# Kernel optimization log

Hardware: AMD Instinct MI355X
Metric: run time of the kernel (lower is better)

The kernel has to match this reference:

```python
import jax, jax.numpy as jnp
import numpy as np

NUM_HEADS = 16
HEAD_DIM = 64

def setup_inputs() -> dict:
    key = jax.random.key(0)
    k1, k2, k3 = jax.random.split(key, 3)
    B, S, H = 2, 2048, 1024
    inner = NUM_HEADS * HEAD_DIM  # 1024
    x = jax.random.normal(k1, (B, S, H), dtype=jnp.float32)
    w_qkv = jax.random.normal(k2, (H, 3 * inner), dtype=jnp.float32) * (1.0 / np.sqrt(H))
    b_qkv = jnp.zeros((3 * inner,), dtype=jnp.float32)
    w_out = jax.random.normal(k3, (inner, H), dtype=jnp.float32) * (1.0 / np.sqrt(inner))
    b_out = jnp.zeros((H,), dtype=jnp.float32)
    return {"x": x, "w_qkv": w_qkv, "b_qkv": b_qkv, "w_out": w_out, "b_out": b_out}

def reference(x, w_qkv, b_qkv, w_out, b_out):
    B, S, H = x.shape
    nh, hd = NUM_HEADS, HEAD_DIM
    qkv = x @ w_qkv + b_qkv                      # [B,S,3*nh*hd]
    qkv = qkv.reshape(B, S, 3, nh, hd)
    qkv = jnp.transpose(qkv, (2, 0, 3, 1, 4))    # [3,B,nh,S,hd]
    q, k, v = qkv[0], qkv[1], qkv[2]
    scale = jnp.sqrt(jnp.asarray(hd, dtype=x.dtype))
    attn = jnp.einsum('bhqd,bhkd->bhqk', q, k) / scale  # [B,nh,S,S]
    attn = jax.nn.softmax(attn, axis=-1)
    out = jnp.einsum('bhqk,bhkd->bhqd', attn, v)        # [B,nh,S,hd]
    out = jnp.transpose(out, (0, 2, 1, 3)).reshape(B, S, nh * hd)
    out = out @ w_out + b_out                    # [B,S,H]
    return out
```

## Files before the change

### kernel.cpp

```cpp
#include <hip/hip_runtime.h>
#include <stdint.h>

typedef short bf16x8 __attribute__((ext_vector_type(8)));
typedef float f32x4 __attribute__((ext_vector_type(4)));

#if __has_builtin(__builtin_amdgcn_exp2f)
#define EXP2F(x) __builtin_amdgcn_exp2f(x)
#else
#define EXP2F(x) exp2f(x)
#endif

#define QSCALE 0.18033688011112042f

__device__ __forceinline__ unsigned short f2bf(float f) {
  unsigned u = __float_as_uint(f);
  u += 0x7fffu + ((u >> 16) & 1u);
  return (unsigned short)(u >> 16);
}

__device__ __forceinline__ unsigned cvtpk(float lo, float hi) {
  unsigned r;
  asm("v_cvt_pk_bf16_f32 %0, %1, %2" : "=v"(r) : "v"(lo), "v"(hi));
  return r;
}

__device__ __forceinline__ void pl32(unsigned& a, unsigned& b) {
  asm("v_permlane32_swap_b32 %0, %1" : "+v"(a), "+v"(b));
}
__device__ __forceinline__ void pl16(unsigned& a, unsigned& b) {
  asm("v_permlane16_swap_b32 %0, %1" : "+v"(a), "+v"(b));
}

__device__ __forceinline__ void gld16(const ushort* g, ushort* l) {
  __builtin_amdgcn_global_load_lds(
      (__attribute__((address_space(1))) void*)g,
      (__attribute__((address_space(3))) void*)l, 16, 0, 0);
}

__global__ __launch_bounds__(256) void k_prep(
    const float* __restrict__ x, ushort* __restrict__ xb,
    const float* __restrict__ wqkv, ushort* __restrict__ wqkvT,
    const float* __restrict__ wout, ushort* __restrict__ woutT) {
  __shared__ float tl[32][33];
  const int t = threadIdx.x;
  const int blk = blockIdx.x;
  if (blk < 2048) {
    int i = (blk * 256 + t) * 8;
    float4 a = *(const float4*)(x + i);
    float4 b = *(const float4*)(x + i + 4);
    union { ushort u[8]; uint4 q; } r;
    r.u[0] = f2bf(a.x); r.u[1] = f2bf(a.y); r.u[2] = f2bf(a.z); r.u[3] = f2bf(a.w);
    r.u[4] = f2bf(b.x); r.u[5] = f2bf(b.y); r.u[6] = f2bf(b.z); r.u[7] = f2bf(b.w);
    *(uint4*)(xb + i) = r.q;
    return;
  }
  const float* in; ushort* out; int C, bx, by;
  if (blk < 5120) {
    int b = blk - 2048; bx = b % 96; by = b / 96;
    in = wqkv; out = wqkvT; C = 3072;
  } else {
    int b = blk - 5120; bx = b & 31; by = b >> 5;
    in = wout; out = woutT; C = 1024;
  }
  const int R = 1024;
  {
    int r = t >> 3, c4 = (t & 7) * 4;
    float4 v = *(const float4*)(in + (size_t)(by * 32 + r) * C + bx * 32 + c4);
    tl[r][c4] = v.x; tl[r][c4 + 1] = v.y; tl[r][c4 + 2] = v.z; tl[r][c4 + 3] = v.w;
  }
  __syncthreads();
  {
    int c = t >> 3, r4 = (t & 7) * 4;
    union { ushort u[4]; uint2 q; } o;
    o.u[0] = f2bf(tl[r4][c]);     o.u[1] = f2bf(tl[r4 + 1][c]);
    o.u[2] = f2bf(tl[r4 + 2][c]); o.u[3] = f2bf(tl[r4 + 3][c]);
    *(uint2*)(out + (size_t)(bx * 32 + c) * R + by * 32 + r4) = o.q;
  }
}

__global__ __launch_bounds__(256, 2) void k_gemm_qkv(
    const ushort* __restrict__ A, const ushort* __restrict__ Bt,
    const float* __restrict__ bias, ushort* __restrict__ Q,
    ushort* __restrict__ Ko, ushort* __restrict__ Vt) {
  __shared__ ushort As[2][128 * 32];
  __shared__ ushort Bs[2][128 * 32];
  const int t = threadIdx.x;
  const int lane = t & 63, wid = t >> 6;
  const int wr = wid >> 1, wc = wid & 1;
  const int rt = blockIdx.y, ct = blockIdx.x;

  const int srow = t >> 2, sslot = t & 3;
  const ushort* ga = A + (size_t)(rt * 128 + srow) * 1024 + sslot * 8;
  const ushort* gb = Bt + (size_t)(ct * 128 + srow) * 1024 + sslot * 8;

  f32x4 acc[4][4];
#pragma unroll
  for (int m = 0; m < 4; ++m)
#pragma unroll
    for (int n = 0; n < 4; ++n) acc[m][n] = (f32x4){0.f, 0.f, 0.f, 0.f};

  int aidx[4], bidx[4];
#pragma unroll
  for (int m = 0; m < 4; ++m) {
    int ra = wr * 64 + m * 16 + (lane & 15);
    aidx[m] = ra * 32 + ((lane >> 4) << 3);
    int rb = wc * 64 + m * 16 + (lane & 15);
    bidx[m] = rb * 32 + ((lane >> 4) << 3);
  }

  gld16(ga, &As[0][t * 8]); gld16(ga + 65536, &As[0][2048 + t * 8]);
  gld16(gb, &Bs[0][t * 8]); gld16(gb + 65536, &Bs[0][2048 + t * 8]);
  __syncthreads();

  int cur = 0;
  for (int kt = 0; kt < 32; ++kt) {
    if (kt < 31) {
      const ushort* ga2 = ga + (kt + 1) * 32;
      const ushort* gb2 = gb + (kt + 1) * 32;
      gld16(ga2, &As[cur ^ 1][t * 8]); gld16(ga2 + 65536, &As[cur ^ 1][2048 + t * 8]);
      gld16(gb2, &Bs[cur ^ 1][t * 8]); gld16(gb2 + 65536, &Bs[cur ^ 1][2048 + t * 8]);
    }
    bf16x8 af[4], bfv[4];
#pragma unroll
    for (int m = 0; m < 4; ++m) af[m] = *(const bf16x8*)&As[cur][aidx[m]];
#pragma unroll
    for (int n = 0; n < 4; ++n) bfv[n] = *(const bf16x8*)&Bs[cur][bidx[n]];
#pragma unroll
    for (int m = 0; m < 4; ++m)
#pragma unroll
      for (int n = 0; n < 4; ++n)
        acc[m][n] = __builtin_amdgcn_mfma_f32_16x16x32_bf16(af[m], bfv[n], acc[m][n], 0, 0, 0);
    __syncthreads();
    cur ^= 1;
  }

  const int colb = ct * 128 + wc * 64;
  const int rowb = rt * 128 + wr * 64;
#pragma unroll
  for (int n = 0; n < 4; ++n) {
    int col = colb + n * 16 + (lane & 15);
    float bv = bias[col];
    int three = col >> 10, hx = (col >> 6) & 15, d = col & 63;
    if (three == 2) {
#pragma unroll
      for (int m = 0; m < 4; ++m) {
        int r0 = rowb + m * 16 + ((lane >> 4) << 2);
        int b = r0 >> 11, s0 = r0 & 2047;
        int s0p = (s0 & ~56) | (((s0 >> 3) ^ d) & 7) << 3;
        union { ushort u[4]; uint2 q; } o;
#pragma unroll
        for (int r = 0; r < 4; ++r) o.u[r] = f2bf(acc[m][n][r] + bv);
        *(uint2*)&Vt[(size_t)(b * 16 + hx) * 131072 + (size_t)d * 2048 + s0p] = o.q;
      }
    } else if (three == 1) {
#pragma unroll
      for (int m = 0; m < 4; ++m) {
        int r0 = rowb + m * 16 + ((lane >> 4) << 2);
#pragma unroll
        for (int r = 0; r < 4; ++r) {
          int row = r0 + r;
          int b = row >> 11, s = row & 2047;
          int dp = (d & 7) | ((((d >> 3) ^ s) & 7) << 3);
          Ko[(size_t)((b * 16 + hx) * 2048 + s) * 64 + dp] = f2bf(acc[m][n][r] + bv);
        }
      }
    } else {
#pragma unroll
      for (int m = 0; m < 4; ++m) {
        int r0 = rowb + m * 16 + ((lane >> 4) << 2);
#pragma unroll
        for (int r = 0; r < 4; ++r) {
          int row = r0 + r;
          int b = row >> 11, s = row & 2047;
          Q[(size_t)((b * 16 + hx) * 2048 + s) * 64 + d] = f2bf((acc[m][n][r] + bv) * QSCALE);
        }
      }
    }
  }
}

__global__ __launch_bounds__(256, 2) void k_gemm_out(
    const ushort* __restrict__ A, const ushort* __restrict__ Bt,
    const float* __restrict__ bias, float* __restrict__ Out) {
  __shared__ ushort As[2][64 * 32];
  __shared__ ushort Bs[2][128 * 32];
  const int t = threadIdx.x;
  const int lane = t & 63, wid = t >> 6;
  const int wr = wid >> 1, wc = wid & 1;
  const int rt = blockIdx.y, ct = blockIdx.x;

  const int srow = t >> 2, sslot = t & 3;
  const ushort* ga = A + (size_t)(rt * 64 + srow) * 1024 + sslot * 8;
  const ushort* gb = Bt + (size_t)(ct * 128 + srow) * 1024 + sslot * 8;

  f32x4 acc[2][4];
#pragma unroll
  for (int m = 0; m < 2; ++m)
#pragma unroll
    for (int n = 0; n < 4; ++n) acc[m][n] = (f32x4){0.f, 0.f, 0.f, 0.f};

  int aidx[2], bidx[4];
#pragma unroll
  for (int m = 0; m < 2; ++m) {
    int ra = wr * 32 + m * 16 + (lane & 15);
    aidx[m] = ra * 32 + ((lane >> 4) << 3);
  }
#pragma unroll
  for (int n = 0; n < 4; ++n) {
    int rb = wc * 64 + n * 16 + (lane & 15);
    bidx[n] = rb * 32 + ((lane >> 4) << 3);
  }

  gld16(ga, &As[0][t * 8]);
  gld16(gb, &Bs[0][t * 8]); gld16(gb + 65536, &Bs[0][2048 + t * 8]);
  __syncthreads();

  int cur = 0;
  for (int kt = 0; kt < 32; ++kt) {
    if (kt < 31) {
      const ushort* ga2 = ga + (kt + 1) * 32;
      const ushort* gb2 = gb + (kt + 1) * 32;
      gld16(ga2, &As[cur ^ 1][t * 8]);
      gld16(gb2, &Bs[cur ^ 1][t * 8]); gld16(gb2 + 65536, &Bs[cur ^ 1][2048 + t * 8]);
    }
    bf16x8 af[2], bfv[4];
#pragma unroll
    for (int m = 0; m < 2; ++m) af[m] = *(const bf16x8*)&As[cur][aidx[m]];
#pragma unroll
    for (int n = 0; n < 4; ++n) bfv[n] = *(const bf16x8*)&Bs[cur][bidx[n]];
#pragma unroll
    for (int m = 0; m < 2; ++m)
#pragma unroll
      for (int n = 0; n < 4; ++n)
        acc[m][n] = __builtin_amdgcn_mfma_f32_16x16x32_bf16(af[m], bfv[n], acc[m][n], 0, 0, 0);
    __syncthreads();
    cur ^= 1;
  }

  const int colb = ct * 128 + wc * 64;
  const int rowb = rt * 64 + wr * 32;
#pragma unroll
  for (int n = 0; n < 4; ++n) {
    int col = colb + n * 16 + (lane & 15);
    float bv = bias[col];
#pragma unroll
    for (int m = 0; m < 2; ++m) {
      int r0 = rowb + m * 16 + ((lane >> 4) << 2);
#pragma unroll
      for (int r = 0; r < 4; ++r)
        Out[(size_t)(r0 + r) * 1024 + col] = acc[m][n][r] + bv;
    }
  }
}

#define QKT_COMPUTE(KSRC, SD)                                                 \
  {                                                                           \
    _Pragma("unroll")                                                         \
    for (int cb = 0; cb < 2; ++cb)                                            \
      _Pragma("unroll")                                                       \
      for (int n = 0; n < 4; ++n) SD[cb][n] = (f32x4){0.f, 0.f, 0.f, 0.f};    \
    __builtin_amdgcn_s_setprio(1);                                            \
    _Pragma("unroll")                                                         \
    for (int kk = 0; kk < 2; ++kk)                                            \
      _Pragma("unroll")                                                       \
      for (int n = 0; n < 4; ++n) {                                           \
        bf16x8 kf = *(const bf16x8*)&(KSRC)[kidx[n][kk]];                     \
        SD[0][n] = __builtin_amdgcn_mfma_f32_16x16x32_bf16(kf, qf[0][kk], SD[0][n], 0, 0, 0); \
        SD[1][n] = __builtin_amdgcn_mfma_f32_16x16x32_bf16(kf, qf[1][kk], SD[1][n], 0, 0, 0); \
      }                                                                       \
    __builtin_amdgcn_s_setprio(0);                                            \
  }

#define ATTN_ITER(T, SCUR, SNXT)                                              \
  {                                                                           \
    if ((T) < 30) {                                                           \
      _Pragma("unroll")                                                       \
      for (int i = 0; i < 2; ++i) {                                           \
        int row = (wid * 2 + i) * 8 + strow;                                  \
        gld16(&Kh[(size_t)(((T) + 2) * 64 + row) * 64 + stch],                \
              Kstg + (wid * 2 + i) * 512 + lane * 8);                         \
        gld16(&Vh[(size_t)row * 2048 + ((T) + 2) * 64 + stch],                \
              Vstg + (wid * 2 + i) * 512 + lane * 8);                         \
      }                                                                       \
    }                                                                         \
    if ((T) < 31) QKT_COMPUTE(Knxt, SNXT);                                    \
    uint2 W[2][4];                                                            \
    _Pragma("unroll")                                                         \
    for (int cb = 0; cb < 2; ++cb) {                                          \
      float ps = lpart[cb];                                                   \
      _Pragma("unroll")                                                       \
      for (int n = 0; n < 4; ++n) {                                           \
        float p0 = EXP2F(SCUR[cb][n][0] - 16.0f);                             \
        float p1 = EXP2F(SCUR[cb][n][1] - 16.0f);                             \
        float p2 = EXP2F(SCUR[cb][n][2] - 16.0f);                             \
        float p3 = EXP2F(SCUR[cb][n][3] - 16.0f);                             \
        ps += (p0 + p1) + (p2 + p3);                                          \
        W[cb][n].x = cvtpk(p0, p1);                                           \
        W[cb][n].y = cvtpk(p2, p3);                                           \
      }                                                                       \
      lpart[cb] = ps;                                                         \
    }                                                                         \
    __builtin_amdgcn_s_setprio(1);                                            \
    _Pragma("unroll")                                                         \
    for (int kk = 0; kk < 2; ++kk) {                                          \
      bf16x8 paf[2];                                                          \
      _Pragma("unroll")                                                       \
      for (int cb = 0; cb < 2; ++cb) {                                        \
        unsigned a0 = W[cb][2 * kk].x, b0 = W[cb][2 * kk + 1].x;              \
        pl32(a0, b0); pl16(a0, b0);                                           \
        unsigned a1 = W[cb][2 * kk].y, b1 = W[cb][2 * kk + 1].y;              \
        pl32(a1, b1); pl16(a1, b1);                                           \
        union { unsigned u[4]; bf16x8 v; } fr;                                \
        fr.u[0] = a0; fr.u[1] = a1; fr.u[2] = b0; fr.u[3] = b1;               \
        paf[cb] = fr.v;                                                       \
      }                                                                       \
      _Pragma("unroll")                                                       \
      for (int nd = 0; nd < 4; ++nd) {                                        \
        bf16x8 vf = *(const bf16x8*)&Vcur[kidx[nd][kk]];                      \
        oacc[0][nd] = __builtin_amdgcn_mfma_f32_16x16x32_bf16(paf[0], vf, oacc[0][nd], 0, 0, 0); \
        oacc[1][nd] = __builtin_amdgcn_mfma_f32_16x16x32_bf16(paf[1], vf, oacc[1][nd], 0, 0, 0); \
      }                                                                       \
    }                                                                         \
    __builtin_amdgcn_s_setprio(0);                                            \
    __syncthreads();                                                          \
    { ushort* tk = Kcur; Kcur = Knxt; Knxt = Kstg; Kstg = tk;                 \
      ushort* tv = Vcur; Vcur = Vnxt; Vnxt = Vstg; Vstg = tv; }               \
  }

__global__ __launch_bounds__(256, 2) void k_attn(const ushort* __restrict__ Qb,
                                                 const ushort* __restrict__ Kb,
                                                 const ushort* __restrict__ Vtb,
                                                 ushort* __restrict__ AO) {
  __shared__ ushort Ks[3][64 * 64];
  __shared__ ushort Vs[3][64 * 64];
  const int t = threadIdx.x, lane = t & 63, wid = t >> 6;
  const int c = lane & 15, g = lane >> 4;
  const int bh = blockIdx.y, qt = blockIdx.x;
  const ushort* Qh = Qb + (size_t)bh * 131072;
  const ushort* Kh = Kb + (size_t)bh * 131072;
  const ushort* Vh = Vtb + (size_t)bh * 131072;

  bf16x8 qf[2][2];
#pragma unroll
  for (int cb = 0; cb < 2; ++cb)
#pragma unroll
    for (int kk = 0; kk < 2; ++kk) {
      int row = qt * 128 + wid * 32 + cb * 16 + c;
      qf[cb][kk] = *(const bf16x8*)&Qh[row * 64 + kk * 32 + g * 8];
    }

  f32x4 oacc[2][4];
#pragma unroll
  for (int cb = 0; cb < 2; ++cb)
#pragma unroll
    for (int n = 0; n < 4; ++n) oacc[cb][n] = (f32x4){0.f, 0.f, 0.f, 0.f};
  float lpart[2] = {0.f, 0.f};

  const int strow = lane >> 3, stch = (lane & 7) * 8;

  int kidx[4][2];
#pragma unroll
  for (int n = 0; n < 4; ++n)
#pragma unroll
    for (int kk = 0; kk < 2; ++kk)
      kidx[n][kk] = (n * 16 + c) * 64 + (((kk * 4 + g) ^ (c & 7)) << 3);

  ushort *Kcur = &Ks[0][0], *Knxt = &Ks[1][0], *Kstg = &Ks[2][0];
  ushort *Vcur = &Vs[0][0], *Vnxt = &Vs[1][0], *Vstg = &Vs[2][0];

#pragma unroll
  for (int i = 0; i < 2; ++i) {
    int row = (wid * 2 + i) * 8 + strow;
    gld16(&Kh[(size_t)row * 64 + stch], Kcur + (wid * 2 + i) * 512 + lane * 8);
    gld16(&Vh[(size_t)row * 2048 + stch], Vcur + (wid * 2 + i) * 512 + lane * 8);
    gld16(&Kh[(size_t)(64 + row) * 64 + stch], Knxt + (wid * 2 + i) * 512 + lane * 8);
    gld16(&Vh[(size_t)row * 2048 + 64 + stch], Vnxt + (wid * 2 + i) * 512 + lane * 8);
  }
  __syncthreads();

  f32x4 sA[2][4], sB[2][4];
  QKT_COMPUTE(Kcur, sA);

  for (int kt = 0; kt < 32; kt += 2) {
    ATTN_ITER(kt, sA, sB);
    ATTN_ITER(kt + 1, sB, sA);
  }

  const int b = bh >> 4, h = bh & 15;
#pragma unroll
  for (int cb = 0; cb < 2; ++cb) {
    float lp = lpart[cb];
    lp += __shfl_xor(lp, 16);
    lp += __shfl_xor(lp, 32);
    float inv = 1.0f / lp;
    float invr[4];
#pragma unroll
    for (int r = 0; r < 4; ++r) invr[r] = __shfl(inv, (g << 2) + r);
#pragma unroll
    for (int nd = 0; nd < 4; ++nd) {
      int d = nd * 16 + c;
#pragma unroll
      for (int r = 0; r < 4; ++r) {
        int s = qt * 128 + wid * 32 + cb * 16 + (g << 2) + r;
        AO[(size_t)((b * 2048 + s) * 16 + h) * 64 + d] = f2bf(oacc[cb][nd][r] * invr[r]);
      }
    }
  }
}

extern "C" void kernel_launch(void* const* d_in, const int* in_sizes, int n_in,
                              void* d_out, int out_size, void* d_ws, size_t ws_size,
                              hipStream_t stream) {
  const float* x = (const float*)d_in[0];
  const float* w_qkv = (const float*)d_in[1];
  const float* b_qkv = (const float*)d_in[2];
  const float* w_out = (const float*)d_in[3];
  const float* b_out = (const float*)d_in[4];
  float* out = (float*)d_out;

  char* p = (char*)d_ws;
  ushort* xb = (ushort*)p;    p += (size_t)4096 * 1024 * 2;
  ushort* wqkvT = (ushort*)p; p += (size_t)3072 * 1024 * 2;
  ushort* woutT = (ushort*)p; p += (size_t)1024 * 1024 * 2;
  ushort* Qb = (ushort*)p;    p += (size_t)32 * 2048 * 64 * 2;
  ushort* Kb = (ushort*)p;    p += (size_t)32 * 2048 * 64 * 2;
  ushort* Vtb = (ushort*)p;   p += (size_t)32 * 2048 * 64 * 2;
  ushort* AO = xb;

  k_prep<<<6144, 256, 0, stream>>>(x, xb, w_qkv, wqkvT, w_out, woutT);
  k_gemm_qkv<<<dim3(24, 32), 256, 0, stream>>>(xb, wqkvT, b_qkv, Qb, Kb, Vtb);
  k_attn<<<dim3(16, 32), 256, 0, stream>>>(Qb, Kb, Vtb, AO);
  k_gemm_out<<<dim3(8, 64), 256, 0, stream>>>(AO, woutT, b_out, out);
}
```

Before: 109.5 us.

## Deepen LDS prefetch pipelines with vmcnt-gated barriers in GEMMs and attention

```diff
diff --git a/kernel.cpp b/kernel.cpp
--- a/kernel.cpp
+++ b/kernel.cpp
@@ -36,6 +36,14 @@
       (__attribute__((address_space(1))) void*)g,
       (__attribute__((address_space(3))) void*)l, 16, 0, 0);
 }
+
+#define VMBAR(N)                                          \
+  asm volatile("s_waitcnt vmcnt(" #N ")" ::: "memory");   \
+  __builtin_amdgcn_s_barrier();                           \
+  __builtin_amdgcn_sched_barrier(0);
+#define BARONLY                                           \
+  __builtin_amdgcn_s_barrier();                           \
+  __builtin_amdgcn_sched_barrier(0);
 
 __global__ __launch_bounds__(256) void k_prep(
     const float* __restrict__ x, ushort* __restrict__ xb,
@@ -78,12 +86,34 @@
   }
 }
 
+#define QKV_BODY(KT, ISSUE)                                                   \
+  {                                                                           \
+    if (ISSUE) {                                                              \
+      const ushort* ga2 = ga + ((KT) + 2) * 32;                               \
+      const ushort* gb2 = gb + ((KT) + 2) * 32;                               \
+      gld16(ga2, Astg + t * 8); gld16(ga2 + 65536, Astg + 2048 + t * 8);      \
+      gld16(gb2, Bstg + t * 8); gld16(gb2 + 65536, Bstg + 2048 + t * 8);      \
+    }                                                                         \
+    bf16x8 af[4], bfv[4];                                                     \
+    _Pragma("unroll")                                                         \
+    for (int m = 0; m < 4; ++m) af[m] = *(const bf16x8*)&Acur[aidx[m]];       \
+    _Pragma("unroll")                                                         \
+    for (int n = 0; n < 4; ++n) bfv[n] = *(const bf16x8*)&Bcur[bidx[n]];      \
+    _Pragma("unroll")                                                         \
+    for (int m = 0; m < 4; ++m)                                               \
+      _Pragma("unroll")                                                       \
+      for (int n = 0; n < 4; ++n)                                             \
+        acc[m][n] = __builtin_amdgcn_mfma_f32_16x16x32_bf16(af[m], bfv[n], acc[m][n], 0, 0, 0); \
+    { ushort* ta = Acur; Acur = Anxt; Anxt = Astg; Astg = ta;                 \
+      ushort* tb = Bcur; Bcur = Bnxt; Bnxt = Bstg; Bstg = tb; }               \
+  }
+
 __global__ __launch_bounds__(256, 2) void k_gemm_qkv(
     const ushort* __restrict__ A, const ushort* __restrict__ Bt,
     const float* __restrict__ bias, ushort* __restrict__ Q,
     ushort* __restrict__ Ko, ushort* __restrict__ Vt) {
-  __shared__ ushort As[2][128 * 32];
-  __shared__ ushort Bs[2][128 * 32];
+  __shared__ ushort As[3][128 * 32];
+  __shared__ ushort Bs[3][128 * 32];
   const int t = threadIdx.x;
   const int lane = t & 63, wid = t >> 6;
   const int wr = wid >> 1, wc = wid & 1;
@@ -108,31 +138,26 @@
     bidx[m] = rb * 32 + ((lane >> 4) << 3);
   }
 
-  gld16(ga, &As[0][t * 8]); gld16(ga + 65536, &As[0][2048 + t * 8]);
-  gld16(gb, &Bs[0][t * 8]); gld16(gb + 65536, &Bs[0][2048 + t * 8]);
-  __syncthreads();
-
-  int cur = 0;
-  for (int kt = 0; kt < 32; ++kt) {
-    if (kt < 31) {
-      const ushort* ga2 = ga + (kt + 1) * 32;
-      const ushort* gb2 = gb + (kt + 1) * 32;
-      gld16(ga2, &As[cur ^ 1][t * 8]); gld16(ga2 + 65536, &As[cur ^ 1][2048 + t * 8]);
-      gld16(gb2, &Bs[cur ^ 1][t * 8]); gld16(gb2 + 65536, &Bs[cur ^ 1][2048 + t * 8]);
-    }
-    bf16x8 af[4], bfv[4];
-#pragma unroll
-    for (int m = 0; m < 4; ++m) af[m] = *(const bf16x8*)&As[cur][aidx[m]];
-#pragma unroll
-    for (int n = 0; n < 4; ++n) bfv[n] = *(const bf16x8*)&Bs[cur][bidx[n]];
-#pragma unroll
-    for (int m = 0; m < 4; ++m)
-#pragma unroll
-      for (int n = 0; n < 4; ++n)
-        acc[m][n] = __builtin_amdgcn_mfma_f32_16x16x32_bf16(af[m], bfv[n], acc[m][n], 0, 0, 0);
-    __syncthreads();
-    cur ^= 1;
-  }
+  ushort *Acur = &As[0][0], *Anxt = &As[1][0], *Astg = &As[2][0];
+  ushort *Bcur = &Bs[0][0], *Bnxt = &Bs[1][0], *Bstg = &Bs[2][0];
+
+  gld16(ga, Acur + t * 8); gld16(ga + 65536, Acur + 2048 + t * 8);
+  gld16(gb, Bcur + t * 8); gld16(gb + 65536, Bcur + 2048 + t * 8);
+  {
+    const ushort* ga1 = ga + 32;
+    const ushort* gb1 = gb + 32;
+    gld16(ga1, Anxt + t * 8); gld16(ga1 + 65536, Anxt + 2048 + t * 8);
+    gld16(gb1, Bnxt + t * 8); gld16(gb1 + 65536, Bnxt + 2048 + t * 8);
+  }
+  VMBAR(4)
+
+  for (int kt = 0; kt < 30; ++kt) {
+    QKV_BODY(kt, true)
+    VMBAR(4)
+  }
+  QKV_BODY(30, false)
+  VMBAR(0)
+  QKV_BODY(31, false)
 
   const int colb = ct * 128 + wc * 64;
   const int rowb = rt * 128 + wr * 64;
@@ -179,11 +204,33 @@
   }
 }
 
+#define OUT_BODY(KT, ISSUE)                                                   \
+  {                                                                           \
+    if (ISSUE) {                                                              \
+      const ushort* ga2 = ga + ((KT) + 2) * 32;                               \
+      const ushort* gb2 = gb + ((KT) + 2) * 32;                               \
+      gld16(ga2, Astg + t * 8);                                               \
+      gld16(gb2, Bstg + t * 8); gld16(gb2 + 65536, Bstg + 2048 + t * 8);      \
+    }                                                                         \
+    bf16x8 af[2], bfv[4];                                                     \
+    _Pragma("unroll")                                                         \
+    for (int m = 0; m < 2; ++m) af[m] = *(const bf16x8*)&Acur[aidx[m]];       \
+    _Pragma("unroll")                                                         \
+    for (int n = 0; n < 4; ++n) bfv[n] = *(const bf16x8*)&Bcur[bidx[n]];      \
+    _Pragma("unroll")                                                         \
+    for (int m = 0; m < 2; ++m)                                               \
+      _Pragma("unroll")                                                       \
+      for (int n = 0; n < 4; ++n)                                             \
+        acc[m][n] = __builtin_amdgcn_mfma_f32_16x16x32_bf16(af[m], bfv[n], acc[m][n], 0, 0, 0); \
+    { ushort* ta = Acur; Acur = Anxt; Anxt = Astg; Astg = ta;                 \
+      ushort* tb = Bcur; Bcur = Bnxt; Bnxt = Bstg; Bstg = tb; }               \
+  }
+
 __global__ __launch_bounds__(256, 2) void k_gemm_out(
     const ushort* __restrict__ A, const ushort* __restrict__ Bt,
     const float* __restrict__ bias, float* __restrict__ Out) {
-  __shared__ ushort As[2][64 * 32];
-  __shared__ ushort Bs[2][128 * 32];
+  __shared__ ushort As[3][64 * 32];
+  __shared__ ushort Bs[3][128 * 32];
   const int t = threadIdx.x;
   const int lane = t & 63, wid = t >> 6;
   const int wr = wid >> 1, wc = wid & 1;
@@ -211,31 +258,26 @@
     bidx[n] = rb * 32 + ((lane >> 4) << 3);
   }
 
-  gld16(ga, &As[0][t * 8]);
-  gld16(gb, &Bs[0][t * 8]); gld16(gb + 65536, &Bs[0][2048 + t * 8]);
-  __syncthreads();
-
-  int cur = 0;
-  for (int kt = 0; kt < 32; ++kt) {
-    if (kt < 31) {
-      const ushort* ga2 = ga + (kt + 1) * 32;
-      const ushort* gb2 = gb + (kt + 1) * 32;
-      gld16(ga2, &As[cur ^ 1][t * 8]);
-      gld16(gb2, &Bs[cur ^ 1][t * 8]); gld16(gb2 + 65536, &Bs[cur ^ 1][2048 + t * 8]);
-    }
-    bf16x8 af[2], bfv[4];
-#pragma unroll
-    for (int m = 0; m < 2; ++m) af[m] = *(const bf16x8*)&As[cur][aidx[m]];
-#pragma unroll
-    for (int n = 0; n < 4; ++n) bfv[n] = *(const bf16x8*)&Bs[cur][bidx[n]];
-#pragma unroll
-    for (int m = 0; m < 2; ++m)
-#pragma unroll
-      for (int n = 0; n < 4; ++n)
-        acc[m][n] = __builtin_amdgcn_mfma_f32_16x16x32_bf16(af[m], bfv[n], acc[m][n], 0, 0, 0);
-    __syncthreads();
-    cur ^= 1;
-  }
+  ushort *Acur = &As[0][0], *Anxt = &As[1][0], *Astg = &As[2][0];
+  ushort *Bcur = &Bs[0][0], *Bnxt = &Bs[1][0], *Bstg = &Bs[2][0];
+
+  gld16(ga, Acur + t * 8);
+  gld16(gb, Bcur + t * 8); gld16(gb + 65536, Bcur + 2048 + t * 8);
+  {
+    const ushort* ga1 = ga + 32;
+    const ushort* gb1 = gb + 32;
+    gld16(ga1, Anxt + t * 8);
+    gld16(gb1, Bnxt + t * 8); gld16(gb1 + 65536, Bnxt + 2048 + t * 8);
+  }
+  VMBAR(3)
+
+  for (int kt = 0; kt < 30; ++kt) {
+    OUT_BODY(kt, true)
+    VMBAR(3)
+  }
+  OUT_BODY(30, false)
+  VMBAR(0)
+  OUT_BODY(31, false)
 
   const int colb = ct * 128 + wc * 64;
   const int rowb = rt * 64 + wr * 32;
@@ -273,13 +315,13 @@
 
 #define ATTN_ITER(T, SCUR, SNXT)                                              \
   {                                                                           \
-    if ((T) < 30) {                                                           \
+    if ((T) < 29) {                                                           \
       _Pragma("unroll")                                                       \
       for (int i = 0; i < 2; ++i) {                                           \
         int row = (wid * 2 + i) * 8 + strow;                                  \
-        gld16(&Kh[(size_t)(((T) + 2) * 64 + row) * 64 + stch],                \
+        gld16(&Kh[(size_t)(((T) + 3) * 64 + row) * 64 + stch],                \
               Kstg + (wid * 2 + i) * 512 + lane * 8);                         \
-        gld16(&Vh[(size_t)row * 2048 + ((T) + 2) * 64 + stch],                \
+        gld16(&Vh[(size_t)row * 2048 + ((T) + 3) * 64 + stch],                \
               Vstg + (wid * 2 + i) * 512 + lane * 8);                         \
       }                                                                       \
     }                                                                         \
@@ -322,17 +364,16 @@
       }                                                                       \
     }                                                                         \
     __builtin_amdgcn_s_setprio(0);                                            \
-    __syncthreads();                                                          \
-    { ushort* tk = Kcur; Kcur = Knxt; Knxt = Kstg; Kstg = tk;                 \
-      ushort* tv = Vcur; Vcur = Vnxt; Vnxt = Vstg; Vstg = tv; }               \
+    { ushort* tk = Kcur; Kcur = Knxt; Knxt = Kn2; Kn2 = Kstg; Kstg = tk;      \
+      ushort* tv = Vcur; Vcur = Vnxt; Vnxt = Vn2; Vn2 = Vstg; Vstg = tv; }    \
   }
 
 __global__ __launch_bounds__(256, 2) void k_attn(const ushort* __restrict__ Qb,
                                                  const ushort* __restrict__ Kb,
                                                  const ushort* __restrict__ Vtb,
                                                  ushort* __restrict__ AO) {
-  __shared__ ushort Ks[3][64 * 64];
-  __shared__ ushort Vs[3][64 * 64];
+  __shared__ ushort Ks[4][64 * 64];
+  __shared__ ushort Vs[4][64 * 64];
   const int t = threadIdx.x, lane = t & 63, wid = t >> 6;
   const int c = lane & 15, g = lane >> 4;
   const int bh = blockIdx.y, qt = blockIdx.x;
@@ -365,26 +406,34 @@
     for (int kk = 0; kk < 2; ++kk)
       kidx[n][kk] = (n * 16 + c) * 64 + (((kk * 4 + g) ^ (c & 7)) << 3);
 
-  ushort *Kcur = &Ks[0][0], *Knxt = &Ks[1][0], *Kstg = &Ks[2][0];
-  ushort *Vcur = &Vs[0][0], *Vnxt = &Vs[1][0], *Vstg = &Vs[2][0];
-
-#pragma unroll
-  for (int i = 0; i < 2; ++i) {
-    int row = (wid * 2 + i) * 8 + strow;
-    gld16(&Kh[(size_t)row * 64 + stch], Kcur + (wid * 2 + i) * 512 + lane * 8);
-    gld16(&Vh[(size_t)row * 2048 + stch], Vcur + (wid * 2 + i) * 512 + lane * 8);
-    gld16(&Kh[(size_t)(64 + row) * 64 + stch], Knxt + (wid * 2 + i) * 512 + lane * 8);
-    gld16(&Vh[(size_t)row * 2048 + 64 + stch], Vnxt + (wid * 2 + i) * 512 + lane * 8);
-  }
-  __syncthreads();
+  ushort *Kcur = &Ks[0][0], *Knxt = &Ks[1][0], *Kn2 = &Ks[2][0], *Kstg = &Ks[3][0];
+  ushort *Vcur = &Vs[0][0], *Vnxt = &Vs[1][0], *Vn2 = &Vs[2][0], *Vstg = &Vs[3][0];
+
+  {
+    ushort* kb[3] = {Kcur, Knxt, Kn2};
+    ushort* vb[3] = {Vcur, Vnxt, Vn2};
+#pragma unroll
+    for (int tt = 0; tt < 3; ++tt)
+#pragma unroll
+      for (int i = 0; i < 2; ++i) {
+        int row = (wid * 2 + i) * 8 + strow;
+        gld16(&Kh[(size_t)(tt * 64 + row) * 64 + stch], kb[tt] + (wid * 2 + i) * 512 + lane * 8);
+        gld16(&Vh[(size_t)row * 2048 + tt * 64 + stch], vb[tt] + (wid * 2 + i) * 512 + lane * 8);
+      }
+  }
+  VMBAR(4)
 
   f32x4 sA[2][4], sB[2][4];
   QKT_COMPUTE(Kcur, sA);
 
-  for (int kt = 0; kt < 32; kt += 2) {
-    ATTN_ITER(kt, sA, sB);
-    ATTN_ITER(kt + 1, sB, sA);
-  }
+  for (int kt = 0; kt < 28; kt += 2) {
+    ATTN_ITER(kt, sA, sB) VMBAR(4)
+    ATTN_ITER(kt + 1, sB, sA) VMBAR(4)
+  }
+  ATTN_ITER(28, sA, sB) VMBAR(4)
+  ATTN_ITER(29, sB, sA) VMBAR(0)
+  ATTN_ITER(30, sA, sB) BARONLY
+  ATTN_ITER(31, sB, sA)
 
   const int b = bh >> 4, h = bh & 15;
 #pragma unroll
```

Result: slower. 112.4 us (+2.6%).
